# Kernel optimization log

Measured on AMD Instinct MI355X. Metric: run time of the kernel, lower is better.

The kernel has to match this reference:

```python
import jax, jax.numpy as jnp
import numpy as np

M_PARAM = 8          # M from __init__
NUM_INTERESTS = 32   # K, num_extracted_interests (max)


def setup_inputs() -> dict:
    key = jax.random.key(0)
    ks = jax.random.split(key, 6)
    bs, L, N, d, ic, K = 512, 100, 64, 256, 256, NUM_INTERESTS
    history = jax.random.normal(ks[0], (bs, L, d), dtype=jnp.float32)
    history_mask = jnp.ones((bs, L), dtype=bool)  # unused by the original forward, kept for signature fidelity
    candidates = jax.random.normal(ks[1], (bs, N, d), dtype=jnp.float32)
    num_extracted_interests = jnp.maximum(
        jax.random.randint(ks[2], (bs,), 0, K, dtype=jnp.int32), 1)
    unique_category_counts = jax.random.randint(ks[3], (bs,), 1, 19, dtype=jnp.int32)
    W = jax.random.normal(ks[4], (ic, d), dtype=jnp.float32) / np.sqrt(d)   # Linear(news_dim->interest_dim), no bias
    context_codes = jax.random.normal(ks[5], (K, ic), dtype=jnp.float32) / np.sqrt(ic)
    return {
        "history_news_representations": history,
        "history_mask": history_mask,
        "candidate_news_representations": candidates,
        "num_extracted_interests": num_extracted_interests,
        "unique_category_counts": unique_category_counts,
        "W": W,
        "context_codes": context_codes,
    }


def _user_encoder(history, candidates, num_interests, cat_counts, W, context_codes):
    bs, L, d = history.shape
    K = context_codes.shape[0]
    # ---- PolyAttention ----
    proj = jnp.tanh(jnp.einsum('bld,cd->blc', history, W))           # [bs, L, ic]
    scores = jnp.einsum('blc,kc->bkl', proj, context_codes)          # [bs, K, L]
    code_mask = jnp.arange(K)[None, :] < num_interests[:, None]      # [bs, K]
    scores = jnp.where(code_mask[:, :, None], scores, jnp.float32(-1e9))
    attn = jax.nn.softmax(scores, axis=2)                            # over history length L
    attn = jnp.nan_to_num(attn, nan=0.0, posinf=0.0, neginf=0.0)
    interests = jnp.einsum('bkl,bld->bkd', attn, history)            # [bs, K, d]
    # ---- InterestCandidateAttention, vectorized over all N candidates ----
    w = jnp.einsum('bkd,bnd->bnk', interests, candidates)            # [bs, N, K]
    dynK = jnp.clip(
        jnp.ceil(jnp.log2(M_PARAM * cat_counts.astype(jnp.float32))).astype(jnp.int32),
        1, K)                                                        # [bs]
    # variable-K top-k mask via descending ranks (values a.s. distinct)
    order = jnp.argsort(-w, axis=-1)
    ranks = jnp.argsort(order, axis=-1)                              # rank 0 = largest
    topk_mask = (ranks < dynK[:, None, None]).astype(w.dtype)        # [bs, N, K]
    masked = w * topk_mask
    user = jnp.einsum('bnk,bkd->bnd', masked, interests)             # [bs, N, d]
    return user


def reference(history_news_representations, history_mask, candidate_news_representations,
              num_extracted_interests, unique_category_counts, W, context_codes):
    return _user_encoder(history_news_representations, candidate_news_representations,
                         num_extracted_interests, unique_category_counts, W, context_codes)
```

## Files before the change

### kernel.cpp

```cpp
#include <hip/hip_runtime.h>
#include <hip/hip_bf16.h>

typedef __bf16 bf16_t;
typedef __bf16 bf16x8 __attribute__((ext_vector_type(8)));
typedef float  f32x4  __attribute__((ext_vector_type(4)));

#define BS 512
#define LH 100
#define NC 64
#define DD 256
#define IC 256
#define KK 32

#define OFF_WPL 6553600
#define OFF_CPL (6553600 + 3 * 131072)

__device__ __forceinline__ void split3(float v, bf16_t& h, bf16_t& l, bf16_t& l2) {
    h = (bf16_t)v;  float r1 = v - (float)h;
    l = (bf16_t)r1; float r2 = r1 - (float)l;
    l2 = (bf16_t)r2;
}

__device__ __forceinline__ void split3x8(const float* v, bf16x8& h, bf16x8& l, bf16x8& l2) {
#pragma unroll
    for (int j = 0; j < 8; j++) {
        bf16_t a, b, c;
        split3(v[j], a, b, c);
        h[j] = a; l[j] = b; l2[j] = c;
    }
}

__device__ __forceinline__ void mfma6(const bf16x8& ah, const bf16x8& al, const bf16x8& al2,
                                      const bf16x8& bh, const bf16x8& bl, const bf16x8& bl2,
                                      f32x4& accM, f32x4& accC) {
    accM = __builtin_amdgcn_mfma_f32_16x16x32_bf16(ah,  bh,  accM, 0, 0, 0);
    accC = __builtin_amdgcn_mfma_f32_16x16x32_bf16(ah,  bl,  accC, 0, 0, 0);
    accC = __builtin_amdgcn_mfma_f32_16x16x32_bf16(al,  bh,  accC, 0, 0, 0);
    accC = __builtin_amdgcn_mfma_f32_16x16x32_bf16(ah,  bl2, accC, 0, 0, 0);
    accC = __builtin_amdgcn_mfma_f32_16x16x32_bf16(al,  bl,  accC, 0, 0, 0);
    accC = __builtin_amdgcn_mfma_f32_16x16x32_bf16(al2, bh,  accC, 0, 0, 0);
}

__device__ __forceinline__ float fast_tanh_f32(float xf) {
    const double t  = fabs((double)xf) * 2.0;
    const double nf = rint(t * 1.4426950408889634);
    double r = fma(nf, -6.93147180369123816490e-01, t);
    r = fma(nf, -1.90821492927058770002e-10, r);
    const double r2 = r * r;
    double p =        2.08767569878680989792e-09;
    p = fma(p, r,     2.50521083854417187751e-08);
    p = fma(p, r,     2.75573192239858906526e-07);
    p = fma(p, r,     2.75573192239858925110e-06);
    p = fma(p, r,     2.48015873015873015873e-05);
    p = fma(p, r,     1.98412698412698412526e-04);
    p = fma(p, r,     1.38888888888888894069e-03);
    p = fma(p, r,     8.33333333333333321769e-03);
    p = fma(p, r,     4.16666666666666643537e-02);
    p = fma(p, r,     1.66666666666666657415e-01);
    p = fma(p, r,     5.00000000000000000000e-01);
    const double q   = fma(r2, p, r);
    const double s   = ldexp(1.0, (int)nf);
    const double em1 = fma(s, q, s - 1.0);
    double ti = em1 / (em1 + 2.0);
    if (t > 20.0) ti = 1.0;
    return copysignf((float)ti, xf);
}

__global__ __launch_bounds__(256) void kp_split(const float* __restrict__ W,
                                                const float* __restrict__ C,
                                                bf16_t* __restrict__ Wh, bf16_t* __restrict__ Wl,
                                                bf16_t* __restrict__ Wl2,
                                                bf16_t* __restrict__ Ch, bf16_t* __restrict__ Cl,
                                                bf16_t* __restrict__ Cl2) {
    int idx = blockIdx.x * 256 + threadIdx.x;
    if (idx < 65536) {
        bf16_t h, l, l2;
        split3(W[idx], h, l, l2);
        Wh[idx] = h; Wl[idx] = l; Wl2[idx] = l2;
    } else {
        int i = idx - 65536;
        if (i < 8192) {
            bf16_t h, l, l2;
            split3(C[i], h, l, l2);
            Ch[i] = h; Cl[i] = l; Cl2[i] = l2;
        }
    }
}

#define WCH 24576
__global__ __launch_bounds__(448) void k12_proj_scores(const float* __restrict__ H,
                                                       const bf16_t* __restrict__ Wh,
                                                       const bf16_t* __restrict__ Wl,
                                                       const bf16_t* __restrict__ Wl2,
                                                       const bf16_t* __restrict__ Ch,
                                                       const bf16_t* __restrict__ Cl,
                                                       const bf16_t* __restrict__ Cl2,
                                                       float* __restrict__ S) {
    __shared__ __align__(16) char wbuf[2][WCH];
    __shared__ float pl[7][16 * 34];

    const int tid = threadIdx.x;
    const int wave = tid >> 6;
    const int lane = tid & 63;
    const int r = lane & 15, q = lane >> 4;
    const int b = blockIdx.x;
    const int lrow0 = wave * 16;

    const bf16_t* it_base[4];
    int it_src[4], it_dst[4];
#pragma unroll
    for (int it = 0; it < 4; it++) {
        const int g = tid + it * 448;
        const int p = (g >> 9) & 3, rem = g & 511, row = rem >> 5, grp = rem & 31;
        it_base[it] = (p == 0) ? Wh : (p == 1) ? Wl : Wl2;
        it_src[it] = row * DD + grp * 8;
        it_dst[it] = (p * 16 + row) * 512 + ((grp * 16) ^ ((row & 7) << 4));
    }
    const bool has4 = (tid < 192);

    bf16x8 Ah[8], Al[8], Al2[8];
    {
        long grow = (long)b * LH + lrow0 + r;
        const long maxrow = (long)BS * LH - 1;
        if (grow > maxrow) grow = maxrow;
        const float* arow = H + (size_t)grow * DD + q * 8;
#pragma unroll
        for (int ks = 0; ks < 8; ks++) {
            const float* ap = arow + ks * 32;
            float4 u = *(const float4*)ap;
            float4 v = *(const float4*)(ap + 4);
            float av[8] = {u.x, u.y, u.z, u.w, v.x, v.y, v.z, v.w};
            split3x8(av, Ah[ks], Al[ks], Al2[ks]);
        }
    }

    const f32x4 zero = {0.f, 0.f, 0.f, 0.f};
    f32x4 saccM[2], saccC[2];
    saccM[0] = zero; saccM[1] = zero; saccC[0] = zero; saccC[1] = zero;

    float* myp = pl[wave];
    const int swz = (r & 7) << 4;

    {
        bf16x8 p0 = *(const bf16x8*)(it_base[0] + it_src[0]);
        bf16x8 p1 = *(const bf16x8*)(it_base[1] + it_src[1]);
        bf16x8 p2 = *(const bf16x8*)(it_base[2] + it_src[2]);
        bf16x8 p3;
        if (has4) p3 = *(const bf16x8*)(it_base[3] + it_src[3]);
        *(bf16x8*)(wbuf[0] + it_dst[0]) = p0;
        *(bf16x8*)(wbuf[0] + it_dst[1]) = p1;
        *(bf16x8*)(wbuf[0] + it_dst[2]) = p2;
        if (has4) *(bf16x8*)(wbuf[0] + it_dst[3]) = p3;
    }
    __syncthreads();

    for (int c16 = 0; c16 < 16; c16++) {
        const char* cur = wbuf[c16 & 1];
        char* nxt = wbuf[(c16 & 1) ^ 1];
        const bool pfv = (c16 < 15);

        bf16x8 p0, p1, p2, p3;
        if (pfv) {
            const int co = (c16 + 1) * 16 * DD;
            p0 = *(const bf16x8*)(it_base[0] + co + it_src[0]);
            p1 = *(const bf16x8*)(it_base[1] + co + it_src[1]);
            p2 = *(const bf16x8*)(it_base[2] + co + it_src[2]);
            if (has4) p3 = *(const bf16x8*)(it_base[3] + co + it_src[3]);
        }

        f32x4 aM = zero, aC = zero;
#pragma unroll
        for (int ks = 0; ks < 8; ks++) {
            const int colb = (ks * 64 + q * 16) ^ swz;
            const char* rowp = cur + r * 512 + colb;
            bf16x8 bh  = *(const bf16x8*)(rowp);
            bf16x8 bl  = *(const bf16x8*)(rowp + 8192);
            bf16x8 bl2 = *(const bf16x8*)(rowp + 16384);
            mfma6(Ah[ks], Al[ks], Al2[ks], bh, bl, bl2, aM, aC);
        }

        const int colb2 = (c16 & 1) * 16;
#pragma unroll
        for (int i = 0; i < 4; i++) {
            float s1 = aM[i] + aC[i];
            myp[(q * 4 + i) * 34 + colb2 + r] = fast_tanh_f32(s1);
        }

        if (c16 & 1) {
            const int c0 = (c16 >> 1) * 32;
            const float* ps = myp + r * 34 + q * 8;
            float pv[8];
#pragma unroll
            for (int j = 0; j < 8; j++) pv[j] = ps[j];
            bf16x8 ph, plo, pl2;
            split3x8(pv, ph, plo, pl2);
#pragma unroll
            for (int ntS = 0; ntS < 2; ntS++) {
                const size_t base = (size_t)(ntS * 16 + r) * IC + c0 + q * 8;
                bf16x8 ch  = *(const bf16x8*)(Ch  + base);
                bf16x8 cl  = *(const bf16x8*)(Cl  + base);
                bf16x8 cl2 = *(const bf16x8*)(Cl2 + base);
                mfma6(ph, plo, pl2, ch, cl, cl2, saccM[ntS], saccC[ntS]);
            }
        }

        if (pfv) {
            *(bf16x8*)(nxt + it_dst[0]) = p0;
            *(bf16x8*)(nxt + it_dst[1]) = p1;
            *(bf16x8*)(nxt + it_dst[2]) = p2;
            if (has4) *(bf16x8*)(nxt + it_dst[3]) = p3;
        }
        __syncthreads();
    }

#pragma unroll
    for (int ntS = 0; ntS < 2; ntS++)
#pragma unroll
        for (int i = 0; i < 4; i++) {
            const int lrow = lrow0 + q * 4 + i;
            if (lrow < LH)
                S[((size_t)b * LH + lrow) * KK + ntS * 16 + r] = saccM[ntS][i] + saccC[ntS][i];
        }
}

__global__ __launch_bounds__(512) void k3456_fused(const float* __restrict__ Sg,
                                                   const int* __restrict__ ni,
                                                   const int* __restrict__ cc,
                                                   const float* __restrict__ H,
                                                   const float* __restrict__ cand,
                                                   float* __restrict__ out) {
    __shared__ __align__(16) char smem[47616];
    float*  attn_l = (float*)smem;
    float*  ls     = (float*)(smem + 12800);
    double* red    = (double*)(smem + 25600);
    float*  ht     = (float*)(smem + 12800);
    float*  I_l    = (float*)(smem + 12800);
    float*  shw    = (float*)smem;

    const int b = blockIdx.x;
    const int tid = threadIdx.x;
    const int wave = tid >> 6;
    const int lane = tid & 63;
    const int r = lane & 15, q = lane >> 4;
    const f32x4 zero = {0.f, 0.f, 0.f, 0.f};

    {
        const float* Sb = Sg + (size_t)b * LH * KK;
        for (int i = tid; i < LH * KK; i += 512) ls[i] = Sb[i];
        __syncthreads();

        const int k = tid & 31;
        const int grp = tid >> 5;
        const bool act = (grp < 8);
        const int nib = ni[b];

        double vals[13];
        int cnt = 0;
        if (act) {
            double vmax = -1e300;
            for (int l = grp; l < LH; l += 8) {
                double v = (double)ls[l * KK + k];
                vals[cnt++] = v;
                vmax = fmax(vmax, v);
            }
            red[grp * 33 + k] = vmax;
        }
        __syncthreads();
        if (tid < 32) {
            double m = red[k];
            for (int j = 1; j < 8; j++) m = fmax(m, red[j * 33 + k]);
            red[k] = m;
        }
        __syncthreads();
        const double mx = red[k];
        __syncthreads();

        if (act) {
            double s = 0.0;
            for (int i = 0; i < cnt; i++) {
                double e = exp(vals[i] - mx);
                vals[i] = e;
                s += e;
            }
            red[grp * 33 + k] = s;
        }
        __syncthreads();
        if (tid < 32) {
            double t = 0.0;
            for (int j = 0; j < 8; j++) t += red[j * 33 + k];
            red[k] = t;
        }
        __syncthreads();
        const double inv = 1.0 / red[k];

        if (act) {
            float* ab = attn_l + k * LH;
            const bool masked = (k >= nib);
            cnt = 0;
            for (int l = grp; l < LH; l += 8) {
                ab[l] = masked ? 0.01f : (float)(vals[cnt] * inv);
                cnt++;
            }
        }
    }
    __syncthreads();

    {
        const float* Hb = H + (size_t)b * LH * DD;
        const int mtB = wave & 1;
        const int m0B = mtB * 16;

        f32x4 accM[4], accC[4];
#pragma unroll
        for (int jj = 0; jj < 4; jj++) { accM[jj] = zero; accC[jj] = zero; }

        for (int ks = 0; ks < 4; ks++) {
            const int l0c = ks * 32;
            __syncthreads();
            for (int u = tid; u < 32 * 64; u += 512) {
                const int l = u >> 6, dg = u & 63;
                float4 v = {0.f, 0.f, 0.f, 0.f};
                if (l0c + l < LH) v = *(const float4*)(Hb + (size_t)(l0c + l) * DD + dg * 4);
                ht[(dg * 4 + 0) * 34 + l] = v.x;
                ht[(dg * 4 + 1) * 34 + l] = v.y;
                ht[(dg * 4 + 2) * 34 + l] = v.z;
                ht[(dg * 4 + 3) * 34 + l] = v.w;
            }
            __syncthreads();

            float av[8];
#pragma unroll
            for (int j = 0; j < 8; j++) {
                const int l = l0c + q * 8 + j;
                av[j] = (l < LH) ? attn_l[(m0B + r) * LH + l] : 0.f;
            }
            bf16x8 ah, al, al2;
            split3x8(av, ah, al, al2);

#pragma unroll
            for (int jj = 0; jj < 4; jj++) {
                const int job = wave + jj * 8;
                const int nt = job >> 1;
                const int n0 = nt * 16;
                float bv[8];
                const float* hp = ht + (n0 + r) * 34 + q * 8;
#pragma unroll
                for (int j = 0; j < 8; j++) bv[j] = hp[j];
                bf16x8 bh, bl, bl2;
                split3x8(bv, bh, bl, bl2);
                mfma6(ah, al, al2, bh, bl, bl2, accM[jj], accC[jj]);
            }
        }
        __syncthreads();

#pragma unroll
        for (int jj = 0; jj < 4; jj++) {
            const int job = wave + jj * 8;
            const int nt = job >> 1;
            const int n0 = nt * 16;
#pragma unroll
            for (int i = 0; i < 4; i++)
                I_l[(m0B + q * 4 + i) * 260 + n0 + r] = accM[jj][i] + accC[jj][i];
        }
    }
    __syncthreads();

    {
        const float* Cb = cand + (size_t)b * NC * DD;
        const int job = wave;
        const int mt = job >> 1, nt = job & 1;
        const int m0 = mt * 16, n0 = nt * 16;
        f32x4 accM = zero, accC = zero;
#pragma unroll
        for (int ks = 0; ks < 8; ks++) {
            const float* ap = Cb + (size_t)(m0 + r) * DD + ks * 32 + q * 8;
            const float* bp = I_l + (n0 + r) * 260 + ks * 32 + q * 8;
            float4 u1 = *(const float4*)ap;      float4 u2 = *(const float4*)(ap + 4);
            float4 v1 = *(const float4*)bp;      float4 v2 = *(const float4*)(bp + 4);
            float av[8] = {u1.x,u1.y,u1.z,u1.w,u2.x,u2.y,u2.z,u2.w};
            float bv[8] = {v1.x,v1.y,v1.z,v1.w,v2.x,v2.y,v2.z,v2.w};
            bf16x8 ah, al, al2, bh, bl, bl2;
            split3x8(av, ah, al, al2);
            split3x8(bv, bh, bl, bl2);
            mfma6(ah, al, al2, bh, bl, bl2, accM, accC);
        }
#pragma unroll
        for (int i = 0; i < 4; i++) shw[(m0 + q * 4 + i) * 33 + n0 + r] = accM[i] + accC[i];

        __syncthreads();

        if (tid < NC) {
            const int n = tid;
            int c8 = 8 * cc[b];
            int dynK = 32 - __clz(c8 - 1);
            dynK = min(max(dynK, 1), KK);
            float v[KK];
            for (int k = 0; k < KK; k++) v[k] = shw[n * 33 + k];
            for (int k = 0; k < KK; k++) {
                int rank = 0;
                for (int j = 0; j < KK; j++)
                    rank += (v[j] > v[k]) || (v[j] == v[k] && j < k);
                shw[n * 33 + k] = (rank < dynK) ? v[k] : 0.f;
            }
        }
    }
    __syncthreads();

    {
        const int d = tid & 255;
        const int nh = tid >> 8;
        float icol[KK];
#pragma unroll
        for (int k = 0; k < KK; k++) icol[k] = I_l[k * 260 + d];

        const int nend = nh * 32 + 32;
        for (int n = nh * 32; n < nend; n++) {
            const float* wr = shw + n * 33;
            float acc = 0.f;
#pragma unroll
            for (int k = 0; k < KK; k++) acc += wr[k] * icol[k];
            out[((size_t)b * NC + n) * DD + d] = acc;
        }
    }
}

extern "C" void kernel_launch(void* const* d_in, const int* in_sizes, int n_in,
                              void* d_out, int out_size, void* d_ws, size_t ws_size,
                              hipStream_t stream) {
    const float* hist = (const float*)d_in[0];
    const float* cand = (const float*)d_in[2];
    const int* ni = (const int*)d_in[3];
    const int* cc = (const int*)d_in[4];
    const float* W = (const float*)d_in[5];
    const float* C = (const float*)d_in[6];
    float* out = (float*)d_out;

    char* w8 = (char*)d_ws;
    float*  S   = (float*)(w8 + 0);
    bf16_t* Wh  = (bf16_t*)(w8 + OFF_WPL);
    bf16_t* Wl  = (bf16_t*)(w8 + OFF_WPL + 131072);
    bf16_t* Wl2 = (bf16_t*)(w8 + OFF_WPL + 262144);
    bf16_t* Ch  = (bf16_t*)(w8 + OFF_CPL);
    bf16_t* Cl  = (bf16_t*)(w8 + OFF_CPL + 16384);
    bf16_t* Cl2 = (bf16_t*)(w8 + OFF_CPL + 32768);

    kp_split<<<288, 256, 0, stream>>>(W, C, Wh, Wl, Wl2, Ch, Cl, Cl2);
    k12_proj_scores<<<BS, 448, 0, stream>>>(hist, Wh, Wl, Wl2, Ch, Cl, Cl2, S);
    k3456_fused<<<BS, 512, 0, stream>>>(S, ni, cc, hist, cand, out);
}
```

Measured before the change: 251.4 us.

## Split MFMA accumulator chains, use polynomial exp, parallelize top-k ranking over block

Splits the dependent correction MFMA chain into two independent accumulators so consecutive MFMAs stall less on each other. Replaces the library double exp in the softmax with an inline polynomial exp and fully unrolls the fixed-length loops. Spreads the top-k rank computation from 64 threads to all 512 threads, each ranking 4 of the 32 entries, with a barrier before writing back. This adds register pressure and changes the summation order slightly.

```diff
diff --git a/kernel.cpp b/kernel.cpp
--- a/kernel.cpp
+++ b/kernel.cpp
@@ -39,6 +39,17 @@
     accC = __builtin_amdgcn_mfma_f32_16x16x32_bf16(ah,  bl2, accC, 0, 0, 0);
     accC = __builtin_amdgcn_mfma_f32_16x16x32_bf16(al,  bl,  accC, 0, 0, 0);
     accC = __builtin_amdgcn_mfma_f32_16x16x32_bf16(al2, bh,  accC, 0, 0, 0);
+}
+
+__device__ __forceinline__ void mfma6s(const bf16x8& ah, const bf16x8& al, const bf16x8& al2,
+                                       const bf16x8& bh, const bf16x8& bl, const bf16x8& bl2,
+                                       f32x4& accM, f32x4& accC0, f32x4& accC1) {
+    accM  = __builtin_amdgcn_mfma_f32_16x16x32_bf16(ah,  bh,  accM,  0, 0, 0);
+    accC0 = __builtin_amdgcn_mfma_f32_16x16x32_bf16(ah,  bl,  accC0, 0, 0, 0);
+    accC1 = __builtin_amdgcn_mfma_f32_16x16x32_bf16(al,  bh,  accC1, 0, 0, 0);
+    accC0 = __builtin_amdgcn_mfma_f32_16x16x32_bf16(ah,  bl2, accC0, 0, 0, 0);
+    accC1 = __builtin_amdgcn_mfma_f32_16x16x32_bf16(al,  bl,  accC1, 0, 0, 0);
+    accC0 = __builtin_amdgcn_mfma_f32_16x16x32_bf16(al2, bh,  accC0, 0, 0, 0);
 }
 
 __device__ __forceinline__ float fast_tanh_f32(float xf) {
@@ -66,6 +77,27 @@
     return copysignf((float)ti, xf);
 }
 
+__device__ __forceinline__ double fast_exp_f64(double x) {
+    const double nf = rint(x * 1.4426950408889634);
+    double r = fma(nf, -6.93147180369123816490e-01, x);
+    r = fma(nf, -1.90821492927058770002e-10, r);
+    const double r2 = r * r;
+    double p =        2.08767569878680989792e-09;
+    p = fma(p, r,     2.50521083854417187751e-08);
+    p = fma(p, r,     2.75573192239858906526e-07);
+    p = fma(p, r,     2.75573192239858925110e-06);
+    p = fma(p, r,     2.48015873015873015873e-05);
+    p = fma(p, r,     1.98412698412698412526e-04);
+    p = fma(p, r,     1.38888888888888894069e-03);
+    p = fma(p, r,     8.33333333333333321769e-03);
+    p = fma(p, r,     4.16666666666666643537e-02);
+    p = fma(p, r,     1.66666666666666657415e-01);
+    p = fma(p, r,     5.00000000000000000000e-01);
+    const double q = fma(r2, p, r);
+    const double s = ldexp(1.0, (int)nf);
+    return fma(s, q, s);
+}
+
 __global__ __launch_bounds__(256) void kp_split(const float* __restrict__ W,
                                                 const float* __restrict__ C,
                                                 bf16_t* __restrict__ Wh, bf16_t* __restrict__ Wl,
@@ -168,7 +200,7 @@
             if (has4) p3 = *(const bf16x8*)(it_base[3] + co + it_src[3]);
         }
 
-        f32x4 aM = zero, aC = zero;
+        f32x4 aM = zero, aC0 = zero, aC1 = zero;
 #pragma unroll
         for (int ks = 0; ks < 8; ks++) {
             const int colb = (ks * 64 + q * 16) ^ swz;
@@ -176,13 +208,13 @@
             bf16x8 bh  = *(const bf16x8*)(rowp);
             bf16x8 bl  = *(const bf16x8*)(rowp + 8192);
             bf16x8 bl2 = *(const bf16x8*)(rowp + 16384);
-            mfma6(Ah[ks], Al[ks], Al2[ks], bh, bl, bl2, aM, aC);
+            mfma6s(Ah[ks], Al[ks], Al2[ks], bh, bl, bl2, aM, aC0, aC1);
         }
 
         const int colb2 = (c16 & 1) * 16;
 #pragma unroll
         for (int i = 0; i < 4; i++) {
-            float s1 = aM[i] + aC[i];
+            float s1 = aM[i] + aC0[i] + aC1[i];
             myp[(q * 4 + i) * 34 + colb2 + r] = fast_tanh_f32(s1);
         }
 
@@ -255,12 +287,13 @@
         const int nib = ni[b];
 
         double vals[13];
-        int cnt = 0;
         if (act) {
             double vmax = -1e300;
-            for (int l = grp; l < LH; l += 8) {
-                double v = (double)ls[l * KK + k];
-                vals[cnt++] = v;
+#pragma unroll
+            for (int i = 0; i < 13; i++) {
+                const int l = grp + 8 * i;
+                double v = (l < LH) ? (double)ls[l * KK + k] : -1e300;
+                vals[i] = v;
                 vmax = fmax(vmax, v);
             }
             red[grp * 33 + k] = vmax;
@@ -277,10 +310,14 @@
 
         if (act) {
             double s = 0.0;
-            for (int i = 0; i < cnt; i++) {
-                double e = exp(vals[i] - mx);
-                vals[i] = e;
-                s += e;
+#pragma unroll
+            for (int i = 0; i < 13; i++) {
+                const int l = grp + 8 * i;
+                if (l < LH) {
+                    double e = fast_exp_f64(vals[i] - mx);
+                    vals[i] = e;
+                    s += e;
+                }
             }
             red[grp * 33 + k] = s;
         }
@@ -296,10 +333,10 @@
         if (act) {
             float* ab = attn_l + k * LH;
             const bool masked = (k >= nib);
-            cnt = 0;
-            for (int l = grp; l < LH; l += 8) {
-                ab[l] = masked ? 0.01f : (float)(vals[cnt] * inv);
-                cnt++;
+#pragma unroll
+            for (int i = 0; i < 13; i++) {
+                const int l = grp + 8 * i;
+                if (l < LH) ab[l] = masked ? 0.01f : (float)(vals[i] * inv);
             }
         }
     }
@@ -389,19 +426,29 @@
 
         __syncthreads();
 
-        if (tid < NC) {
-            const int n = tid;
+        {
+            const int n = tid & 63;
+            const int kg = tid >> 6;
             int c8 = 8 * cc[b];
             int dynK = 32 - __clz(c8 - 1);
             dynK = min(max(dynK, 1), KK);
             float v[KK];
-            for (int k = 0; k < KK; k++) v[k] = shw[n * 33 + k];
-            for (int k = 0; k < KK; k++) {
+#pragma unroll
+            for (int j = 0; j < KK; j++) v[j] = shw[n * 33 + j];
+            float keep[4];
+#pragma unroll
+            for (int j = 0; j < 4; j++) {
+                const int kk2 = kg + 8 * j;
                 int rank = 0;
-                for (int j = 0; j < KK; j++)
-                    rank += (v[j] > v[k]) || (v[j] == v[k] && j < k);
-                shw[n * 33 + k] = (rank < dynK) ? v[k] : 0.f;
-            }
+#pragma unroll
+                for (int jj = 0; jj < KK; jj++)
+                    rank += (v[jj] > v[kk2]) || (v[jj] == v[kk2] && jj < kk2);
+                keep[j] = (rank < dynK) ? v[kk2] : 0.f;
+            }
+            __syncthreads();
+#pragma unroll
+            for (int j = 0; j < 4; j++)
+                shw[n * 33 + kg + 8 * j] = keep[j];
         }
     }
     __syncthreads();
```

Result: faster. 232.0 us (-7.7%).
